# Kernel tuning notes

Hardware: AMD Instinct MI355X
Metric: run time of the kernel (lower is better)

Reference implementation:

```python
import jax, jax.numpy as jnp
import numpy as np

N_NODES = 100000


def _gcn_layer(x, W, b, src, dst, dinv):
    # x: [N, din]; W: [din, dout]; src/dst: [E+N] (self-loops included); dinv: [N]
    h = x @ W                                   # [N, dout] small GEMM
    norm = dinv[src] * dinv[dst]                # [E+N]
    msg = h[src] * norm[:, None]                # [E+N, dout] gather
    out = jax.ops.segment_sum(msg, dst, num_segments=N_NODES)  # scatter-add
    return jax.nn.relu(out + b)


def setup_inputs() -> dict:
    key = jax.random.key(0)
    ks = jax.random.split(key, 8)
    d_in, d_h = 128, 128
    x = jax.random.normal(ks[0], (N_NODES, d_in), dtype=jnp.float32)
    edge_index = jax.random.randint(ks[1], (2, 1600000), 0, N_NODES, dtype=jnp.int64)
    def glorot(k, din, dout):
        lim = np.sqrt(6.0 / (din + dout)).astype(np.float32)
        return jax.random.uniform(k, (din, dout), jnp.float32, -lim, lim)
    W1 = glorot(ks[2], d_in, d_h); b1 = jnp.zeros((d_h,), jnp.float32)
    W2 = glorot(ks[3], d_h, d_h); b2 = jnp.zeros((d_h,), jnp.float32)
    W3 = glorot(ks[4], d_h, d_h); b3 = jnp.zeros((d_h,), jnp.float32)
    return {"x": x, "W1": W1, "b1": b1, "W2": W2, "b2": b2,
            "W3": W3, "b3": b3, "edge_index": edge_index}


def reference(x, W1, b1, W2, b2, W3, b3, edge_index):
    # GCNConv (Kipf & Welling): D^{-1/2}(A+I)D^{-1/2} X W + b, per layer, with ReLU.
    loop = jnp.arange(N_NODES, dtype=edge_index.dtype)
    src = jnp.concatenate([edge_index[0], loop])  # self-loops appended
    dst = jnp.concatenate([edge_index[1], loop])
    deg = jax.ops.segment_sum(jnp.ones_like(dst, dtype=x.dtype), dst,
                              num_segments=N_NODES)
    dinv = jnp.where(deg > 0, jax.lax.rsqrt(deg), 0.0)
    h = _gcn_layer(x, W1, b1, src, dst, dinv)
    h = _gcn_layer(h, W2, b2, src, dst, dinv)
    h = _gcn_layer(h, W3, b3, src, dst, dinv)
    return h
```

## Files before the change

### kernel.cpp

```cpp
#include <hip/hip_runtime.h>
#include <hip/hip_fp16.h>
#include <math.h>

#define NN 100000
#define DD 128
#define SCAN_CHUNK 2048
#define AGG_BLOCKS 2048

typedef short short8 __attribute__((ext_vector_type(8)));
typedef float f32x4 __attribute__((ext_vector_type(4)));

__global__ __launch_bounds__(256) void hist_rank_kernel(const int* __restrict__ dst, int E,
                                                        int* __restrict__ deg,
                                                        int* __restrict__ rank) {
    int i = blockIdx.x * 256 + threadIdx.x;
    int e = i * 4;
    if (e + 3 < E) {
        int4 d4 = ((const int4*)dst)[i];
        int4 r4;
        r4.x = atomicAdd(&deg[d4.x], 1);
        r4.y = atomicAdd(&deg[d4.y], 1);
        r4.z = atomicAdd(&deg[d4.z], 1);
        r4.w = atomicAdd(&deg[d4.w], 1);
        ((int4*)rank)[i] = r4;
    } else {
        for (; e < E; ++e) rank[e] = atomicAdd(&deg[dst[e]], 1);
    }
}

__global__ __launch_bounds__(256) void scan1_kernel(const int* __restrict__ deg,
                                                    int* __restrict__ chunkSum,
                                                    float* __restrict__ dinv, int n) {
    __shared__ int lds[256];
    int tid = threadIdx.x;
    int base = blockIdx.x * SCAN_CHUNK + tid * 8;
    int s = 0;
    #pragma unroll
    for (int j = 0; j < 8; ++j) {
        int idx = base + j;
        if (idx < n) {
            int d = deg[idx];
            s += d;
            dinv[idx] = rsqrtf((float)d + 1.0f);
        }
    }
    lds[tid] = s;
    __syncthreads();
    for (int d = 128; d > 0; d >>= 1) {
        if (tid < d) lds[tid] += lds[tid + d];
        __syncthreads();
    }
    if (tid == 0) chunkSum[blockIdx.x] = lds[0];
}

__global__ void scan2_kernel(int* __restrict__ chunkSum, int* __restrict__ chunkOff,
                             int nb, int* __restrict__ offsets) {
    __shared__ int lds[512];
    int tid = threadIdx.x;
    if (tid < nb) lds[tid] = chunkSum[tid];
    __syncthreads();
    if (tid == 0) {
        int run = 0;
        for (int i = 0; i < nb; ++i) {
            int v = lds[i];
            lds[i] = run;
            run += v;
        }
        offsets[NN] = run;
    }
    __syncthreads();
    if (tid < nb) chunkOff[tid] = lds[tid];
}

__global__ __launch_bounds__(256) void scan3_kernel(const int* __restrict__ deg,
                                                    const int* __restrict__ chunkOff,
                                                    int* __restrict__ offsets, int n) {
    __shared__ int lds[256];
    int tid = threadIdx.x;
    int base = blockIdx.x * SCAN_CHUNK + tid * 8;
    int v[8];
    int tsum = 0;
    #pragma unroll
    for (int j = 0; j < 8; ++j) {
        int idx = base + j;
        v[j] = (idx < n) ? deg[idx] : 0;
        tsum += v[j];
    }
    lds[tid] = tsum;
    __syncthreads();
    for (int d = 1; d < 256; d <<= 1) {
        int t = (tid >= d) ? lds[tid - d] : 0;
        __syncthreads();
        lds[tid] += t;
        __syncthreads();
    }
    int excl = lds[tid] - tsum;
    int off0 = chunkOff[blockIdx.x] + excl;
    int run = 0;
    #pragma unroll
    for (int j = 0; j < 8; ++j) {
        int idx = base + j;
        if (idx < n) offsets[idx] = off0 + run;
        run += v[j];
    }
}

__global__ __launch_bounds__(256) void fill_kernel(const int* __restrict__ src,
                                                   const int* __restrict__ dst,
                                                   const int* __restrict__ rank, int E,
                                                   const int* __restrict__ offsets,
                                                   int* __restrict__ csr) {
    int i = blockIdx.x * 256 + threadIdx.x;
    int e = i * 4;
    if (e + 3 < E) {
        int4 d4 = ((const int4*)dst)[i];
        int4 s4 = ((const int4*)src)[i];
        int4 r4 = ((const int4*)rank)[i];
        int o0 = offsets[d4.x];
        int o1 = offsets[d4.y];
        int o2 = offsets[d4.z];
        int o3 = offsets[d4.w];
        csr[o0 + r4.x] = s4.x;
        csr[o1 + r4.y] = s4.y;
        csr[o2 + r4.z] = s4.z;
        csr[o3 + r4.w] = s4.w;
    } else {
        for (; e < E; ++e) csr[offsets[dst[e]] + rank[e]] = src[e];
    }
}

__device__ __forceinline__ unsigned short f2bf(float f) {
    unsigned int u = __float_as_uint(f);
    unsigned int r = u + 0x7FFFu + ((u >> 16) & 1u);
    return (unsigned short)(r >> 16);
}

__device__ __forceinline__ void split8(const float* v, short8& hi, short8& lo) {
    #pragma unroll
    for (int j = 0; j < 8; ++j) {
        float f = v[j];
        unsigned short h = f2bf(f);
        float fl = f - __uint_as_float(((unsigned int)h) << 16);
        hi[j] = (short)h;
        lo[j] = (short)f2bf(fl);
    }
}

__global__ __launch_bounds__(256) void wsplit3_kernel(const float* __restrict__ W1,
                                                      const float* __restrict__ W2,
                                                      const float* __restrict__ W3,
                                                      uint4* __restrict__ wh,
                                                      uint4* __restrict__ wl) {
    int b = blockIdx.x;
    int layer = b >> 3;
    const float* W = (layer == 0) ? W1 : (layer == 1) ? W2 : W3;
    int i = (b & 7) * 256 + threadIdx.x;
    int lane_e = i & 63;
    int ks = (i >> 6) & 3;
    int cf = i >> 8;
    int colb = cf * 16 + (lane_e & 15);
    int rowb = ks * 32 + (lane_e >> 4) * 8;
    float wvv[8];
    #pragma unroll
    for (int j = 0; j < 8; ++j) wvv[j] = W[(rowb + j) * DD + colb];
    short8 h, l;
    split8(wvv, h, l);
    union { short8 s; uint4 u; } ch, cl;
    ch.s = h; cl.s = l;
    wh[layer * 2048 + i] = ch.u;
    wl[layer * 2048 + i] = cl.u;
}

template <typename InT>
__global__ __launch_bounds__(256, 2) void gemm_norm_kernel(
    const InT* __restrict__ X, const uint4* __restrict__ whg,
    const uint4* __restrict__ wlg,
    const float* __restrict__ dinv, __half* __restrict__ G)
{
    __shared__ uint4 whf[2048];
    __shared__ uint4 wlf[2048];

    const int tid  = threadIdx.x;
    const int base = blockIdx.x * 128;
    const int lane = tid & 63;
    const int wv   = tid >> 6;
    const int kg   = lane >> 4;
    const int mcol = lane & 15;

    #pragma unroll
    for (int p = 0; p < 8; ++p) {
        int i = tid + p * 256;
        whf[i] = whg[i];
        wlf[i] = wlg[i];
    }

    short8 ah[2][4], al[2][4];
    #pragma unroll
    for (int rf = 0; rf < 2; ++rf) {
        int arow = base + wv * 32 + rf * 16 + mcol;
        if (arow >= NN) arow = NN - 1;
        const InT* xr = X + (size_t)arow * DD;
        #pragma unroll
        for (int ks = 0; ks < 4; ++ks) {
            int k0 = ks * 32 + kg * 8;
            float av[8];
            if constexpr (sizeof(InT) == 4) {
                *(float4*)&av[0] = *(const float4*)&xr[k0];
                *(float4*)&av[4] = *(const float4*)&xr[k0 + 4];
            } else {
                union { uint4 u; __half h[8]; } hv;
                hv.u = *(const uint4*)&xr[k0];
                #pragma unroll
                for (int j = 0; j < 8; ++j) av[j] = __half2float(hv.h[j]);
            }
            split8(av, ah[rf][ks], al[rf][ks]);
        }
    }
    __syncthreads();

    #pragma unroll 1
    for (int cf = 0; cf < 8; ++cf) {
        f32x4 acc0 = {0.f, 0.f, 0.f, 0.f};
        f32x4 acc1 = {0.f, 0.f, 0.f, 0.f};
        #pragma unroll
        for (int ks = 0; ks < 4; ++ks) {
            union { uint4 u; short8 s; } bh, bl;
            bh.u = whf[(cf * 4 + ks) * 64 + lane];
            bl.u = wlf[(cf * 4 + ks) * 64 + lane];
            acc0 = __builtin_amdgcn_mfma_f32_16x16x32_bf16(ah[0][ks], bh.s, acc0, 0, 0, 0);
            acc0 = __builtin_amdgcn_mfma_f32_16x16x32_bf16(al[0][ks], bh.s, acc0, 0, 0, 0);
            acc0 = __builtin_amdgcn_mfma_f32_16x16x32_bf16(ah[0][ks], bl.s, acc0, 0, 0, 0);
            acc1 = __builtin_amdgcn_mfma_f32_16x16x32_bf16(ah[1][ks], bh.s, acc1, 0, 0, 0);
            acc1 = __builtin_amdgcn_mfma_f32_16x16x32_bf16(al[1][ks], bh.s, acc1, 0, 0, 0);
            acc1 = __builtin_amdgcn_mfma_f32_16x16x32_bf16(ah[1][ks], bl.s, acc1, 0, 0, 0);
        }
        #pragma unroll
        for (int rf = 0; rf < 2; ++rf) {
            const f32x4 acc = rf ? acc1 : acc0;
            int row0 = base + wv * 32 + rf * 16 + kg * 4;
            if (row0 < NN) {
                float dv[4];
                *(float4*)dv = *(const float4*)&dinv[row0];
                #pragma unroll
                for (int j = 0; j < 4; ++j) {
                    G[(size_t)(row0 + j) * DD + cf * 16 + mcol] =
                        __float2half(acc[j] * dv[j]);
                }
            }
        }
    }
}

__device__ __forceinline__ float4 gload(const __half* __restrict__ g, int idx, int cq) {
    uint2 u = *(const uint2*)(g + (size_t)idx * DD + cq * 4);
    __half2 h0 = *reinterpret_cast<const __half2*>(&u.x);
    __half2 h1 = *reinterpret_cast<const __half2*>(&u.y);
    float2 f0 = __half22float2(h0);
    float2 f1 = __half22float2(h1);
    return make_float4(f0.x, f0.y, f1.x, f1.y);
}

template <typename OutT>
__global__ __launch_bounds__(256) void agg_kernel(
    const __half* __restrict__ g, const float* __restrict__ dinv,
    const int* __restrict__ off, const int* __restrict__ csr,
    const float* __restrict__ bias, OutT* __restrict__ out)
{
    const int wid  = threadIdx.x >> 6;
    const int lane = threadIdx.x & 63;
    const int sub  = lane >> 5;
    const int cq   = lane & 31;
    const float4 bb = ((const float4*)bias)[cq];
    const int ngroups = (NN + 3) / 4;

    for (int grp = blockIdx.x; grp < ngroups; grp += AGG_BLOCKS) {
        int node = grp * 4 + wid;
        if (node >= NN) continue;

        float4 acc = make_float4(0.f, 0.f, 0.f, 0.f);
        float4 acc2 = make_float4(0.f, 0.f, 0.f, 0.f);
        if (sub == 0) acc = gload(g, node, cq);

        const int e0 = off[node], end = off[node + 1];
        const int cnt = end - e0;
        const int pairs = cnt >> 1;
        const int np4 = pairs & ~3;

        if (np4) {
            int i0 = csr[e0 + 0 + sub];
            int i1 = csr[e0 + 2 + sub];
            int i2 = csr[e0 + 4 + sub];
            int i3 = csr[e0 + 6 + sub];
            for (int p = 4; p < np4; p += 4) {
                int b0 = e0 + 2 * p + sub;
                int j0 = csr[b0];
                int j1 = csr[b0 + 2];
                int j2 = csr[b0 + 4];
                int j3 = csr[b0 + 6];
                float4 v0 = gload(g, i0, cq);
                float4 v1 = gload(g, i1, cq);
                float4 v2 = gload(g, i2, cq);
                float4 v3 = gload(g, i3, cq);
                acc.x += v0.x + v2.x; acc.y += v0.y + v2.y;
                acc.z += v0.z + v2.z; acc.w += v0.w + v2.w;
                acc2.x += v1.x + v3.x; acc2.y += v1.y + v3.y;
                acc2.z += v1.z + v3.z; acc2.w += v1.w + v3.w;
                i0 = j0; i1 = j1; i2 = j2; i3 = j3;
            }
            float4 v0 = gload(g, i0, cq);
            float4 v1 = gload(g, i1, cq);
            float4 v2 = gload(g, i2, cq);
            float4 v3 = gload(g, i3, cq);
            acc.x += v0.x + v2.x; acc.y += v0.y + v2.y;
            acc.z += v0.z + v2.z; acc.w += v0.w + v2.w;
            acc2.x += v1.x + v3.x; acc2.y += v1.y + v3.y;
            acc2.z += v1.z + v3.z; acc2.w += v1.w + v3.w;
        }
        for (int q = np4; q < pairs; ++q) {
            int s = csr[e0 + 2 * q + sub];
            float4 v = gload(g, s, cq);
            acc.x += v.x; acc.y += v.y; acc.z += v.z; acc.w += v.w;
        }
        if ((cnt & 1) && sub == 0) {
            int s = csr[end - 1];
            float4 v = gload(g, s, cq);
            acc.x += v.x; acc.y += v.y; acc.z += v.z; acc.w += v.w;
        }

        acc.x += acc2.x; acc.y += acc2.y; acc.z += acc2.z; acc.w += acc2.w;
        acc.x += __shfl_xor(acc.x, 32, 64);
        acc.y += __shfl_xor(acc.y, 32, 64);
        acc.z += __shfl_xor(acc.z, 32, 64);
        acc.w += __shfl_xor(acc.w, 32, 64);

        if (sub == 0) {
            float di = dinv[node];
            float4 o;
            o.x = fmaxf(fmaf(acc.x, di, bb.x), 0.f);
            o.y = fmaxf(fmaf(acc.y, di, bb.y), 0.f);
            o.z = fmaxf(fmaf(acc.z, di, bb.z), 0.f);
            o.w = fmaxf(fmaf(acc.w, di, bb.w), 0.f);
            if constexpr (sizeof(OutT) == 4) {
                ((float4*)out)[(size_t)node * 32 + cq] = o;
            } else {
                uint2 st;
                __half2 h0 = __floats2half2_rn(o.x, o.y);
                __half2 h1 = __floats2half2_rn(o.z, o.w);
                st.x = *reinterpret_cast<unsigned int*>(&h0);
                st.y = *reinterpret_cast<unsigned int*>(&h1);
                *(uint2*)((__half*)out + (size_t)node * DD + cq * 4) = st;
            }
        }
    }
}

extern "C" void kernel_launch(void* const* d_in, const int* in_sizes, int n_in,
                              void* d_out, int out_size, void* d_ws, size_t ws_size,
                              hipStream_t stream)
{
    const float* x  = (const float*)d_in[0];
    const float* W1 = (const float*)d_in[1];
    const float* b1 = (const float*)d_in[2];
    const float* W2 = (const float*)d_in[3];
    const float* b2 = (const float*)d_in[4];
    const float* W3 = (const float*)d_in[5];
    const float* b3 = (const float*)d_in[6];
    const int*   ei = (const int*)d_in[7];

    const int E = in_sizes[7] / 2;
    const int* src = ei;
    const int* dst = ei + E;

    float* out = (float*)d_out;

    char* wsb = (char*)d_ws;
    size_t p = 0;
    int* deg      = (int*)(wsb + p); p += ((size_t)NN * 4 + 1023) & ~1023ull;
    int* offsets  = (int*)(wsb + p); p += ((size_t)(NN + 1) * 4 + 1023) & ~1023ull;
    int* chunkSum = (int*)(wsb + p); p += 4096;
    int* chunkOff = (int*)(wsb + p); p += 4096;
    int* csr      = (int*)(wsb + p); p += ((size_t)E * 4 + 1023) & ~1023ull;
    int* rank     = (int*)(wsb + p); p += ((size_t)E * 4 + 1023) & ~1023ull;
    float* dinv   = (float*)(wsb + p); p += ((size_t)NN * 4 + 1023) & ~1023ull;
    uint4* wh     = (uint4*)(wsb + p); p += 3 * 2048 * sizeof(uint4);
    uint4* wl     = (uint4*)(wsb + p); p += 3 * 2048 * sizeof(uint4);
    __half* g     = (__half*)(wsb + p); p += (size_t)NN * DD * 2;
    __half* h_act = (__half*)(wsb + p); p += (size_t)NN * DD * 2;

    const int NB = (NN + SCAN_CHUNK - 1) / SCAN_CHUNK;

    hipMemsetAsync(deg, 0, (size_t)NN * 4, stream);
    hist_rank_kernel<<<(E / 4 + 256) / 256 + 1, 256, 0, stream>>>(dst, E, deg, rank);
    scan1_kernel<<<NB, 256, 0, stream>>>(deg, chunkSum, dinv, NN);
    scan2_kernel<<<1, 512, 0, stream>>>(chunkSum, chunkOff, NB, offsets);
    scan3_kernel<<<NB, 256, 0, stream>>>(deg, chunkOff, offsets, NN);
    fill_kernel<<<(E / 4 + 256) / 256 + 1, 256, 0, stream>>>(src, dst, rank, E, offsets, csr);
    wsplit3_kernel<<<24, 256, 0, stream>>>(W1, W2, W3, wh, wl);

    const int gemm_grid = (NN + 127) / 128;

    gemm_norm_kernel<float><<<gemm_grid, 256, 0, stream>>>(x, wh, wl, dinv, g);
    agg_kernel<__half><<<AGG_BLOCKS, 256, 0, stream>>>(g, dinv, offsets, csr, b1, h_act);
    gemm_norm_kernel<__half><<<gemm_grid, 256, 0, stream>>>(h_act, wh + 2048, wl + 2048, dinv, g);
    agg_kernel<__half><<<AGG_BLOCKS, 256, 0, stream>>>(g, dinv, offsets, csr, b2, h_act);
    gemm_norm_kernel<__half><<<gemm_grid, 256, 0, stream>>>(h_act, wh + 4096, wl + 4096, dinv, g);
    agg_kernel<float><<<AGG_BLOCKS, 256, 0, stream>>>(g, dinv, offsets, csr, b3, out);
}
```

Before: 388.3 us.

## Transpose MFMA operands in GCN GEMM to vectorize stores and drop LDS staging

The GEMM now swaps the MFMA A/B operands so each lane's accumulator holds four consecutive features of one node. This allows packed half2 8-byte stores and a single per-node dinv load instead of scattered 2-byte stores. The weight tiles are read straight from global memory (L1/L2) instead of being staged in shared memory, which removes the LDS copy and the barrier and relaxes the occupancy hint. The bf16 split also changes from round-to-nearest to truncation via byte permutes; the residual still captures the remainder, so accuracy should hold but rounding differs slightly.

```diff
diff --git a/kernel.cpp b/kernel.cpp
--- a/kernel.cpp
+++ b/kernel.cpp
@@ -146,6 +146,27 @@
     }
 }
 
+__device__ __forceinline__ void split8t(const float* v, short8& hi, short8& lo) {
+    const unsigned int* u = (const unsigned int*)v;
+    float lof[8];
+    #pragma unroll
+    for (int j = 0; j < 8; ++j)
+        lof[j] = v[j] - __uint_as_float(u[j] & 0xFFFF0000u);
+    const unsigned int* lu = (const unsigned int*)lof;
+    union { short8 s; unsigned int w[4]; } H, L;
+    #pragma unroll
+    for (int q = 0; q < 4; ++q) {
+#if __has_builtin(__builtin_amdgcn_perm)
+        H.w[q] = __builtin_amdgcn_perm(u[2 * q + 1], u[2 * q], 0x07060302u);
+        L.w[q] = __builtin_amdgcn_perm(lu[2 * q + 1], lu[2 * q], 0x07060302u);
+#else
+        H.w[q] = (u[2 * q + 1] & 0xFFFF0000u) | (u[2 * q] >> 16);
+        L.w[q] = (lu[2 * q + 1] & 0xFFFF0000u) | (lu[2 * q] >> 16);
+#endif
+    }
+    hi = H.s; lo = L.s;
+}
+
 __global__ __launch_bounds__(256) void wsplit3_kernel(const float* __restrict__ W1,
                                                       const float* __restrict__ W2,
                                                       const float* __restrict__ W3,
@@ -172,14 +193,11 @@
 }
 
 template <typename InT>
-__global__ __launch_bounds__(256, 2) void gemm_norm_kernel(
+__global__ __launch_bounds__(256) void gemm_norm_kernel(
     const InT* __restrict__ X, const uint4* __restrict__ whg,
     const uint4* __restrict__ wlg,
     const float* __restrict__ dinv, __half* __restrict__ G)
 {
-    __shared__ uint4 whf[2048];
-    __shared__ uint4 wlf[2048];
-
     const int tid  = threadIdx.x;
     const int base = blockIdx.x * 128;
     const int lane = tid & 63;
@@ -187,17 +205,13 @@
     const int kg   = lane >> 4;
     const int mcol = lane & 15;
 
-    #pragma unroll
-    for (int p = 0; p < 8; ++p) {
-        int i = tid + p * 256;
-        whf[i] = whg[i];
-        wlf[i] = wlg[i];
-    }
-
-    short8 ah[2][4], al[2][4];
+    const int node0 = base + wv * 32 + mcol;
+    const int node1 = node0 + 16;
+
+    short8 xh[2][4], xl[2][4];
     #pragma unroll
     for (int rf = 0; rf < 2; ++rf) {
-        int arow = base + wv * 32 + rf * 16 + mcol;
+        int arow = rf ? node1 : node0;
         if (arow >= NN) arow = NN - 1;
         const InT* xr = X + (size_t)arow * DD;
         #pragma unroll
@@ -213,10 +227,11 @@
                 #pragma unroll
                 for (int j = 0; j < 8; ++j) av[j] = __half2float(hv.h[j]);
             }
-            split8(av, ah[rf][ks], al[rf][ks]);
-        }
-    }
-    __syncthreads();
+            split8t(av, xh[rf][ks], xl[rf][ks]);
+        }
+    }
+    const float di0 = dinv[node0 < NN ? node0 : NN - 1];
+    const float di1 = dinv[node1 < NN ? node1 : NN - 1];
 
     #pragma unroll 1
     for (int cf = 0; cf < 8; ++cf) {
@@ -225,28 +240,31 @@
         #pragma unroll
         for (int ks = 0; ks < 4; ++ks) {
             union { uint4 u; short8 s; } bh, bl;
-            bh.u = whf[(cf * 4 + ks) * 64 + lane];
-            bl.u = wlf[(cf * 4 + ks) * 64 + lane];
-            acc0 = __builtin_amdgcn_mfma_f32_16x16x32_bf16(ah[0][ks], bh.s, acc0, 0, 0, 0);
-            acc0 = __builtin_amdgcn_mfma_f32_16x16x32_bf16(al[0][ks], bh.s, acc0, 0, 0, 0);
-            acc0 = __builtin_amdgcn_mfma_f32_16x16x32_bf16(ah[0][ks], bl.s, acc0, 0, 0, 0);
-            acc1 = __builtin_amdgcn_mfma_f32_16x16x32_bf16(ah[1][ks], bh.s, acc1, 0, 0, 0);
-            acc1 = __builtin_amdgcn_mfma_f32_16x16x32_bf16(al[1][ks], bh.s, acc1, 0, 0, 0);
-            acc1 = __builtin_amdgcn_mfma_f32_16x16x32_bf16(ah[1][ks], bl.s, acc1, 0, 0, 0);
-        }
-        #pragma unroll
-        for (int rf = 0; rf < 2; ++rf) {
-            const f32x4 acc = rf ? acc1 : acc0;
-            int row0 = base + wv * 32 + rf * 16 + kg * 4;
-            if (row0 < NN) {
-                float dv[4];
-                *(float4*)dv = *(const float4*)&dinv[row0];
-                #pragma unroll
-                for (int j = 0; j < 4; ++j) {
-                    G[(size_t)(row0 + j) * DD + cf * 16 + mcol] =
-                        __float2half(acc[j] * dv[j]);
-                }
-            }
+            bh.u = whg[(cf * 4 + ks) * 64 + lane];
+            bl.u = wlg[(cf * 4 + ks) * 64 + lane];
+            acc0 = __builtin_amdgcn_mfma_f32_16x16x32_bf16(bh.s, xh[0][ks], acc0, 0, 0, 0);
+            acc0 = __builtin_amdgcn_mfma_f32_16x16x32_bf16(bl.s, xh[0][ks], acc0, 0, 0, 0);
+            acc0 = __builtin_amdgcn_mfma_f32_16x16x32_bf16(bh.s, xl[0][ks], acc0, 0, 0, 0);
+            acc1 = __builtin_amdgcn_mfma_f32_16x16x32_bf16(bh.s, xh[1][ks], acc1, 0, 0, 0);
+            acc1 = __builtin_amdgcn_mfma_f32_16x16x32_bf16(bl.s, xh[1][ks], acc1, 0, 0, 0);
+            acc1 = __builtin_amdgcn_mfma_f32_16x16x32_bf16(bh.s, xl[1][ks], acc1, 0, 0, 0);
+        }
+        const int fb = cf * 16 + kg * 4;
+        if (node0 < NN) {
+            __half2 p0 = __floats2half2_rn(acc0[0] * di0, acc0[1] * di0);
+            __half2 p1 = __floats2half2_rn(acc0[2] * di0, acc0[3] * di0);
+            uint2 st;
+            st.x = *reinterpret_cast<unsigned int*>(&p0);
+            st.y = *reinterpret_cast<unsigned int*>(&p1);
+            *(uint2*)&G[(size_t)node0 * DD + fb] = st;
+        }
+        if (node1 < NN) {
+            __half2 p0 = __floats2half2_rn(acc1[0] * di1, acc1[1] * di1);
+            __half2 p1 = __floats2half2_rn(acc1[2] * di1, acc1[3] * di1);
+            uint2 st;
+            st.x = *reinterpret_cast<unsigned int*>(&p0);
+            st.y = *reinterpret_cast<unsigned int*>(&p1);
+            *(uint2*)&G[(size_t)node1 * DD + fb] = st;
         }
     }
 }
```

Measured after the change: 392.0 us. About the same (+0.9%).
